# Kernel optimization log

Hardware: AMD Instinct MI355X
Metric: run time of the kernel (lower is better)

The kernel has to match this reference:

```python
import jax, jax.numpy as jnp
import numpy as np

# Dimensions (Gemma-2B-like, uniform q-head rank)
B, S, HID = 2, 2048, 2048
H, HKV, D = 16, 8, 128
RQ, RK, RV = 64, 64, 64
G = H // HKV  # heads per kv group
SCALE = D ** -0.5
NEG_INF = -1e9


def setup_inputs() -> dict:
    key = jax.random.key(0)
    ks = jax.random.split(key, 9)
    hidden_states = jax.random.normal(ks[0], (B, S, HID), dtype=jnp.float32)
    W_A_q = jax.random.normal(ks[1], (H * RQ, HID), dtype=jnp.float32) * 0.02
    W_A_k = jax.random.normal(ks[2], (HKV * RK, HID), dtype=jnp.float32) * 0.02
    W_A_v = jax.random.normal(ks[3], (HKV * RV, HID), dtype=jnp.float32) * 0.02
    B_q = jax.random.normal(ks[4], (H, RQ, D), dtype=jnp.float32)
    B_k = jax.random.normal(ks[5], (HKV, RK, D), dtype=jnp.float32)
    B_v = jax.random.normal(ks[6], (HKV, RV, D), dtype=jnp.float32)
    W_o = jax.random.normal(ks[7], (HID, H * D), dtype=jnp.float32) * 0.02
    # RoPE tables (cos/sin form of gemma's complex freqs_cis)
    inv_freq = 1.0 / (10000.0 ** (jnp.arange(0, D, 2, dtype=jnp.float32) / D))
    freqs = jnp.arange(S, dtype=jnp.float32)[:, None] * inv_freq[None, :]  # [S, D/2]
    freqs_cos = jnp.cos(freqs)
    freqs_sin = jnp.sin(freqs)
    # Causal additive mask [1, 1, S, S]
    causal = jnp.tril(jnp.ones((S, S), dtype=bool))
    mask = jnp.where(causal, 0.0, NEG_INF).astype(jnp.float32)[None, None]
    kv_write_indices = jnp.arange(S, dtype=jnp.int32)
    return {
        'hidden_states': hidden_states, 'W_A_q': W_A_q, 'W_A_k': W_A_k,
        'W_A_v': W_A_v, 'B_q': B_q, 'B_k': B_k, 'B_v': B_v, 'W_o': W_o,
        'freqs_cos': freqs_cos, 'freqs_sin': freqs_sin, 'mask': mask,
        'kv_write_indices': kv_write_indices,
    }


def _rope(x, cos, sin):
    # x: [b, s, h, d]; gemma pairs first half with second half of head_dim
    x1, x2 = jnp.split(x, 2, axis=-1)
    c = cos[None, :, None, :]
    s = sin[None, :, None, :]
    return jnp.concatenate([x1 * c - x2 * s, x1 * s + x2 * c], axis=-1)


def reference(hidden_states, W_A_q, W_A_k, W_A_v, B_q, B_k, B_v, W_o,
              freqs_cos, freqs_sin, mask, kv_write_indices):
    b, s, _ = hidden_states.shape
    # Low-rank A factors
    A_q = jnp.einsum('bsd,rd->bsr', hidden_states, W_A_q).reshape(b, s, H, RQ)
    A_k = jnp.einsum('bsd,rd->bsr', hidden_states, W_A_k).reshape(b, s, HKV, RK)
    A_v = jnp.einsum('bsd,rd->bsr', hidden_states, W_A_v).reshape(b, s, HKV, RV)
    # Factorized KV cache: scatter A factors at write indices (prefill)
    cache_kA = jnp.zeros((b, s, HKV, RK), hidden_states.dtype).at[:, kv_write_indices].set(A_k)
    cache_vA = jnp.zeros((b, s, HKV, RV), hidden_states.dtype).at[:, kv_write_indices].set(A_v)
    # GQA expansion of cached A factors
    gidx = jnp.repeat(jnp.arange(HKV), G)  # [H]
    A_k_rep = cache_kA[:, :, gidx]  # [b, kv, H, RK]
    A_v_rep = cache_vA[:, :, gidx]
    # Reconstruct Q/K/V from constant B factors (per-head loop vectorized:
    # all q ranks equal, so einsum over heads is the same math)
    q = jnp.einsum('bshr,hrd->bshd', A_q, B_q) / RQ
    k = jnp.einsum('bkhr,hrd->bkhd', A_k_rep, B_k[gidx]) / RK
    v = jnp.einsum('bkhr,hrd->bkhd', A_v_rep, B_v[gidx]) / RV
    # RoPE post-reconstruction
    q = _rope(q, freqs_cos, freqs_sin)
    k = _rope(k, freqs_cos, freqs_sin)
    # Attention
    scores = jnp.einsum('bqhd,bkhd->bhqk', q, k) * SCALE + mask
    probs = jax.nn.softmax(scores, axis=-1)
    out = jnp.einsum('bhqk,bkhd->bqhd', probs, v).reshape(b, s, H * D)
    return jnp.einsum('bse,he->bsh', out, W_o)
```

## Files before the change

kernel.cpp:

```cpp
#include <hip/hip_runtime.h>
#include <hip/hip_bf16.h>

typedef __attribute__((ext_vector_type(8))) short bf16x8;
typedef __attribute__((ext_vector_type(4))) float f32x4;

#define MFMA_16x16x32(a,b,c) __builtin_amdgcn_mfma_f32_16x16x32_bf16((a),(b),(c),0,0,0)

__device__ __forceinline__ unsigned short f2b(float f){
  unsigned int u = __builtin_bit_cast(unsigned int, f);
  u = u + 0x7FFFu + ((u >> 16) & 1u);
  return (unsigned short)(u >> 16);
}
__device__ __forceinline__ float b2f(unsigned short h){
  unsigned int u = ((unsigned int)h) << 16;
  return __builtin_bit_cast(float, u);
}

__device__ __forceinline__ void gload_lds16(const unsigned short* g, unsigned short* l){
  __builtin_amdgcn_global_load_lds(
      (const __attribute__((address_space(1))) void*)g,
      (__attribute__((address_space(3))) void*)l, 16, 0, 0);
}


__global__ void cvt_all(const float* __restrict__ hid, const float* __restrict__ wq,
                        const float* __restrict__ wk, const float* __restrict__ wv,
                        const float* __restrict__ wo,
                        unsigned short* __restrict__ Xb, unsigned short* __restrict__ Wqkv,
                        unsigned short* __restrict__ Wob){
  const int N0 = 2097152, N1 = 524288, N2 = 262144, N3 = 262144, N4 = 1048576;
  const int E1 = N0 + N1, E2 = E1 + N2, E3 = E2 + N3, E4 = E3 + N4;
  int i = blockIdx.x * blockDim.x + threadIdx.x;
  const int stride = gridDim.x * blockDim.x;
  for (; i < E4; i += stride){
    const float* s; unsigned short* d; int off;
    if (i < N0)      { s = hid; d = Xb;   off = i; }
    else if (i < E1) { s = wq;  d = Wqkv; off = i - N0; }
    else if (i < E2) { s = wk;  d = Wqkv; off = i - E1 + 524288;  s = wk;  }
    else if (i < E3) { s = wv;  d = Wqkv; off = i - E2 + 786432; }
    else             { s = wo;  d = Wob;  off = i - E3; }
    int src_off = (i < N0) ? i : (i < E1) ? (i - N0) : (i < E2) ? (i - E1) : (i < E3) ? (i - E2) : (i - E3);
    float4 v = reinterpret_cast<const float4*>(s)[src_off];
    ushort4 o;
    o.x = f2b(v.x); o.y = f2b(v.y); o.z = f2b(v.z); o.w = f2b(v.w);
    reinterpret_cast<ushort4*>(d)[off] = o;
  }
}

__global__ void cvt_factors(const float* __restrict__ Bq, const float* __restrict__ Bk,
                            const float* __restrict__ Bv,
                            unsigned short* __restrict__ Bqt, unsigned short* __restrict__ Bkt,
                            unsigned short* __restrict__ Bvt){
  int i = blockIdx.x * blockDim.x + threadIdx.x;
  if (i >= 32*8192) return;
  int H = i >> 13, e = i & 8191;
  int d = e & 127, r = (e >> 7) & 63;
  const float* src; unsigned short* dst; int h;
  if (H < 16)      { src = Bq; dst = Bqt; h = H; }
  else if (H < 24) { src = Bk; dst = Bkt; h = H - 16; }
  else             { src = Bv; dst = Bvt; h = H - 24; }
  dst[(h << 13) + (d << 6) + r] = f2b(src[(size_t)(h << 13) + e]);
}


template<int OUT_F32>
__global__ __launch_bounds__(256) void gemm_bt(
    const unsigned short* __restrict__ A, const unsigned short* __restrict__ B,
    void* __restrict__ Cv, int N, int K, float scale)
{
  __shared__ unsigned short As[2][128*64];
  __shared__ unsigned short Bs[2][128*64];
  const int tid = threadIdx.x;
  const int mb = blockIdx.x, nb = blockIdx.y;
  const int w = tid >> 6, lane = tid & 63;
  const int wr = w >> 1, wc = w & 1;
  const int l16 = lane & 15, lg = lane >> 4;

  f32x4 acc[4][4] = {};

  const unsigned short* Ap = A + (size_t)(mb*128)*K;
  const unsigned short* Bp = B + (size_t)(nb*128)*K;

  const int sRo = 32*w + (lane >> 3);
  const int sCo = ((lane & 7) ^ (lane >> 3)) << 3;
  const int ldsW = 2048*w;

  auto stage = [&](int kt, int buf){
    const unsigned short* Ak = Ap + (size_t)kt*64 + sCo;
    const unsigned short* Bk = Bp + (size_t)kt*64 + sCo;
    #pragma unroll
    for (int i = 0; i < 4; i++)
      gload_lds16(Ak + (size_t)(sRo + 8*i)*K, &As[buf][ldsW + 512*i]);
    #pragma unroll
    for (int i = 0; i < 4; i++)
      gload_lds16(Bk + (size_t)(sRo + 8*i)*K, &Bs[buf][ldsW + 512*i]);
  };

  const int nkt = K >> 6;
  stage(0, 0);
  __syncthreads();

  int cur = 0;
  for (int kt = 0; kt < nkt; kt++){
    if (kt + 1 < nkt) stage(kt + 1, cur ^ 1);
    #pragma unroll
    for (int t = 0; t < 2; t++){
      bf16x8 af[4], bf[4];
      #pragma unroll
      for (int i = 0; i < 4; i++){
        int rowA = wr*64 + i*16 + l16;
        int col  = t*32 + lg*8;
        af[i] = *reinterpret_cast<const bf16x8*>(&As[cur][(rowA*64 + col) ^ ((rowA & 7) << 3)]);
        int rowB = wc*64 + i*16 + l16;
        bf[i] = *reinterpret_cast<const bf16x8*>(&Bs[cur][(rowB*64 + col) ^ ((rowB & 7) << 3)]);
      }
      #pragma unroll
      for (int i = 0; i < 4; i++)
        #pragma unroll
        for (int j = 0; j < 4; j++)
          acc[i][j] = MFMA_16x16x32(af[i], bf[j], acc[i][j]);
    }
    __syncthreads();
    cur ^= 1;
  }

  #pragma unroll
  for (int i = 0; i < 4; i++){
    #pragma unroll
    for (int j = 0; j < 4; j++){
      int row = mb*128 + wr*64 + i*16 + lg*4;
      int col = nb*128 + wc*64 + j*16 + l16;
      #pragma unroll
      for (int r = 0; r < 4; r++){
        float v = acc[i][j][r] * scale;
        if (OUT_F32) reinterpret_cast<float*>(Cv)[(size_t)(row + r)*N + col] = v;
        else reinterpret_cast<unsigned short*>(Cv)[(size_t)(row + r)*N + col] = f2b(v);
      }
    }
  }
}


__global__ __launch_bounds__(256) void factor_rope(
    const unsigned short* __restrict__ A,
    const unsigned short* __restrict__ Bqt, const unsigned short* __restrict__ Bkt,
    const unsigned short* __restrict__ Bvt,
    unsigned short* __restrict__ qb, unsigned short* __restrict__ kb2,
    unsigned short* __restrict__ vb,
    const float* __restrict__ fc, const float* __restrict__ fs)
{
  __shared__ unsigned short As[128*64];
  __shared__ unsigned short Bs[128*64];
  const int tid = threadIdx.x, mb = blockIdx.x, H = blockIdx.y;
  const int w = tid >> 6, lane = tid & 63;
  const int l16 = lane & 15, lg = lane >> 4;
  const float SCALE = 0.08838834764831845f;

  int h, coloff, Hn; const unsigned short* Bt; unsigned short* Out; float scale; bool rope;
  if (H < 16)      { h = H;      coloff = h*64;        Hn = 16; Bt = Bqt + (size_t)h*8192; Out = qb;  scale = SCALE/64.f; rope = true; }
  else if (H < 24) { h = H - 16; coloff = 1024 + h*64; Hn = 8;  Bt = Bkt + (size_t)h*8192; Out = kb2; scale = 1.f/64.f;   rope = true; }
  else             { h = H - 24; coloff = 1536 + h*64; Hn = 8;  Bt = Bvt + (size_t)h*8192; Out = vb;  scale = 1.f/64.f;   rope = false; }

  const int srow = tid >> 3;
  const int scol = (tid & 7) << 3;
  const unsigned short* Ap = A + (size_t)(mb*128)*2048 + coloff;

  #pragma unroll
  for (int c = 0; c < 4; c++){
    int r = srow + 32*c;
    int idx = (r*64 + scol) ^ ((r & 7) << 3);
    *reinterpret_cast<bf16x8*>(&As[idx]) = *reinterpret_cast<const bf16x8*>(Ap + (size_t)r*2048 + scol);
    *reinterpret_cast<bf16x8*>(&Bs[idx]) = *reinterpret_cast<const bf16x8*>(Bt + r*64 + scol);
  }
  __syncthreads();

  f32x4 acc[2][8] = {};
  #pragma unroll
  for (int t = 0; t < 2; t++){
    bf16x8 af[2], bf[8];
    #pragma unroll
    for (int i = 0; i < 2; i++){
      int rowA = w*32 + i*16 + l16;
      int col  = t*32 + lg*8;
      af[i] = *reinterpret_cast<const bf16x8*>(&As[(rowA*64 + col) ^ ((rowA & 7) << 3)]);
    }
    #pragma unroll
    for (int j = 0; j < 8; j++){
      int rowB = j*16 + l16;
      int col  = t*32 + lg*8;
      bf[j] = *reinterpret_cast<const bf16x8*>(&Bs[(rowB*64 + col) ^ ((rowB & 7) << 3)]);
    }
    #pragma unroll
    for (int i = 0; i < 2; i++)
      #pragma unroll
      for (int j = 0; j < 8; j++)
        acc[i][j] = MFMA_16x16x32(af[i], bf[j], acc[i][j]);
  }

  #pragma unroll
  for (int i = 0; i < 2; i++){
    #pragma unroll
    for (int j = 0; j < 4; j++){
      int d = j*16 + l16;
      #pragma unroll
      for (int r = 0; r < 4; r++){
        int row = mb*128 + w*32 + i*16 + lg*4 + r;
        int s = row & 2047, bb = row >> 11;
        float lo = acc[i][j][r] * scale;
        float hi = acc[i][j+4][r] * scale;
        float o1, o2;
        if (rope){
          float cc = fc[(size_t)s*64 + d];
          float ss = fs[(size_t)s*64 + d];
          o1 = lo*cc - hi*ss;
          o2 = lo*ss + hi*cc;
        } else { o1 = lo; o2 = hi; }
        size_t base = ((size_t)(bb*Hn + h)*2048 + s)*128;
        Out[base + d]      = f2b(o1);
        Out[base + 64 + d] = f2b(o2);
      }
    }
  }
}


__device__ __forceinline__ int vt_idx(int d, int kv){
  return d*64 + ((((kv >> 3) + d + (d >> 3)) & 7) << 3) + (kv & 7);
}

__global__ __launch_bounds__(256) void flash_attn(
    const unsigned short* __restrict__ Q,
    const unsigned short* __restrict__ Kb,
    const unsigned short* __restrict__ Vb,
    unsigned short* __restrict__ O)
{
  __shared__ unsigned short Ks[64*128];
  __shared__ unsigned short Vrow[64*128];
  __shared__ unsigned short Vt[128*64];
  __shared__ unsigned short Pl[4][16*64];

  const int tid = threadIdx.x;
  const int w = tid >> 6, lane = tid & 63;
  const int l16 = lane & 15, lg = lane >> 4;
  const int h = blockIdx.y, b = blockIdx.z;
  const int hkv = h >> 1;

  const size_t hbase  = ((size_t)(b*16 + h))*2048*128;
  const size_t kvbase = ((size_t)(b*8 + hkv))*2048*128;

  const int sR = w*16 + (lane >> 4);
  const int sC = (lane & 15) * 8;

  auto stage = [&](int kb){
    #pragma unroll
    for (int i = 0; i < 4; i++){
      int R = sR + i*4;
      const unsigned short* gk = Kb + kvbase + (size_t)(kb*64 + R)*128 + (sC ^ ((R & 7) << 3));
      gload_lds16(gk, &Ks[(w*16 + i*4)*128]);
      const unsigned short* gv = Vb + kvbase + (size_t)(kb*64 + R)*128 + sC;
      gload_lds16(gv, &Vrow[(w*16 + i*4)*128]);
    }
  };

  stage(0);
  __syncthreads();

  const int tkv0 = (tid >> 4) * 4;
  const int td0  = (tid & 15) * 8;

  const int qtiles[2] = { (int)blockIdx.x, 31 - (int)blockIdx.x };

  for (int ph = 0; ph < 2; ph++){
    const int qe = qtiles[ph];
    const size_t qbase = hbase + (size_t)(qe*64 + w*16)*128;
    const int qrow0 = qe*64 + w*16 + lg*4;

    bf16x8 aq[4];
    #pragma unroll
    for (int t = 0; t < 4; t++)
      aq[t] = *reinterpret_cast<const bf16x8*>(&Q[qbase + (size_t)l16*128 + t*32 + lg*8]);

    f32x4 oac[8] = {};
    float mrow[4], lrow[4];
    #pragma unroll
    for (int r = 0; r < 4; r++){ mrow[r] = -1e30f; lrow[r] = 0.f; }

    for (int kb = 0; kb <= qe; kb++){
      bf16x8 vr0 = *reinterpret_cast<const bf16x8*>(&Vrow[(tkv0 + 0)*128 + td0]);
      bf16x8 vr1 = *reinterpret_cast<const bf16x8*>(&Vrow[(tkv0 + 1)*128 + td0]);
      bf16x8 vr2 = *reinterpret_cast<const bf16x8*>(&Vrow[(tkv0 + 2)*128 + td0]);
      bf16x8 vr3 = *reinterpret_cast<const bf16x8*>(&Vrow[(tkv0 + 3)*128 + td0]);

      f32x4 sac[4] = {};
      #pragma unroll
      for (int nt = 0; nt < 4; nt++){
        #pragma unroll
        for (int t = 0; t < 4; t++){
          int rowK = nt*16 + l16;
          int col  = t*32 + lg*8;
          bf16x8 bk = *reinterpret_cast<const bf16x8*>(&Ks[(rowK*128 + col) ^ ((rowK & 7) << 3)]);
          sac[nt] = MFMA_16x16x32(aq[t], bk, sac[nt]);
        }
      }

      #pragma unroll
      for (int j = 0; j < 8; j++){
        unsigned int lo = (unsigned int)(unsigned short)vr0[j] | ((unsigned int)(unsigned short)vr1[j] << 16);
        unsigned int hi = (unsigned int)(unsigned short)vr2[j] | ((unsigned int)(unsigned short)vr3[j] << 16);
        uint2 u; u.x = lo; u.y = hi;
        *reinterpret_cast<uint2*>(&Vt[vt_idx(td0 + j, tkv0)]) = u;
      }

      if (kb == qe){
        #pragma unroll
        for (int nt = 0; nt < 4; nt++){
          int kcol = kb*64 + nt*16 + l16;
          #pragma unroll
          for (int r = 0; r < 4; r++)
            if (kcol > qrow0 + r) sac[nt][r] = -1e30f;
        }
      }
      float corr[4];
      #pragma unroll
      for (int r = 0; r < 4; r++){
        float v = fmaxf(fmaxf(sac[0][r], sac[1][r]), fmaxf(sac[2][r], sac[3][r]));
        v = fmaxf(v, __shfl_xor(v, 1));
        v = fmaxf(v, __shfl_xor(v, 2));
        v = fmaxf(v, __shfl_xor(v, 4));
        v = fmaxf(v, __shfl_xor(v, 8));
        float mn = fmaxf(mrow[r], v);
        corr[r] = __expf(mrow[r] - mn);
        mrow[r] = mn;
      }
      float rs[4] = {0.f, 0.f, 0.f, 0.f};
      #pragma unroll
      for (int nt = 0; nt < 4; nt++){
        #pragma unroll
        for (int r = 0; r < 4; r++){
          float p = __expf(sac[nt][r] - mrow[r]);
          sac[nt][r] = p;
          rs[r] += p;
        }
      }
      #pragma unroll
      for (int r = 0; r < 4; r++){
        float v = rs[r];
        v += __shfl_xor(v, 1); v += __shfl_xor(v, 2); v += __shfl_xor(v, 4); v += __shfl_xor(v, 8);
        lrow[r] = lrow[r]*corr[r] + v;
      }
      #pragma unroll
      for (int dn = 0; dn < 8; dn++)
        #pragma unroll
        for (int r = 0; r < 4; r++) oac[dn][r] *= corr[r];

      #pragma unroll
      for (int nt = 0; nt < 4; nt++){
        #pragma unroll
        for (int r = 0; r < 4; r++){
          int row = lg*4 + r, col = nt*16 + l16;
          Pl[w][(row*64 + col) ^ ((row & 7) << 3)] = f2b(sac[nt][r]);
        }
      }

      __syncthreads();
      if (kb < qe) stage(kb + 1);
      else if (ph == 0) stage(0);

      #pragma unroll
      for (int t = 0; t < 2; t++){
        int colp = t*32 + lg*8;
        bf16x8 ap = *reinterpret_cast<const bf16x8*>(&Pl[w][(l16*64 + colp) ^ ((l16 & 7) << 3)]);
        #pragma unroll
        for (int dn = 0; dn < 8; dn++){
          int rowV = dn*16 + l16;
          bf16x8 bv = *reinterpret_cast<const bf16x8*>(&Vt[vt_idx(rowV, colp)]);
          oac[dn] = MFMA_16x16x32(ap, bv, oac[dn]);
        }
      }
      __syncthreads();
    }

    #pragma unroll
    for (int dn = 0; dn < 8; dn++){
      #pragma unroll
      for (int r = 0; r < 4; r++){
        int row = qe*64 + w*16 + lg*4 + r;
        O[((size_t)(b*2048 + row))*2048 + h*128 + dn*16 + l16] = f2b(oac[dn][r] / lrow[r]);
      }
    }
  }
}


extern "C" void kernel_launch(void* const* d_in, const int* in_sizes, int n_in,
                              void* d_out, int out_size, void* d_ws, size_t ws_size,
                              hipStream_t stream)
{
  if (n_in < 10) return;
  const float* hidden = (const float*)d_in[0];
  const float* WAq = (const float*)d_in[1];
  const float* WAk = (const float*)d_in[2];
  const float* WAv = (const float*)d_in[3];
  const float* Bq  = (const float*)d_in[4];
  const float* Bk  = (const float*)d_in[5];
  const float* Bv  = (const float*)d_in[6];
  const float* Wo  = (const float*)d_in[7];
  const float* fcos = (const float*)d_in[8];
  const float* fsin = (const float*)d_in[9];
  float* out = (float*)d_out;

  char* p = (char*)d_ws;
  auto take = [&](size_t bytes){ char* q = p; p += (bytes + 255) & ~(size_t)255; return q; };
  unsigned short* Xb   = (unsigned short*)take((size_t)4096*2048*2);
  unsigned short* Wqkv = (unsigned short*)take((size_t)2048*2048*2);
  unsigned short* Wob  = (unsigned short*)take((size_t)2048*2048*2);
  unsigned short* Aqkv = (unsigned short*)take((size_t)4096*2048*2);
  unsigned short* Bqt  = (unsigned short*)take((size_t)16*128*64*2);
  unsigned short* Bkt  = (unsigned short*)take((size_t)8*128*64*2);
  unsigned short* Bvt  = (unsigned short*)take((size_t)8*128*64*2);
  unsigned short* qbuf = (unsigned short*)take((size_t)2*16*2048*128*2);
  unsigned short* kbuf = (unsigned short*)take((size_t)2*8*2048*128*2);
  unsigned short* vbuf = (unsigned short*)take((size_t)2*8*2048*128*2);
  unsigned short* aout = (unsigned short*)take((size_t)4096*2048*2);
  if ((size_t)(p - (char*)d_ws) > ws_size) return;

  cvt_all<<<4096, 256, 0, stream>>>(hidden, WAq, WAk, WAv, Wo, Xb, Wqkv, Wob);
  cvt_factors<<<1024, 256, 0, stream>>>(Bq, Bk, Bv, Bqt, Bkt, Bvt);

  gemm_bt<0><<<dim3(32,16), 256, 0, stream>>>(Xb, Wqkv, (void*)Aqkv, 2048, 2048, 1.0f);

  factor_rope<<<dim3(32,32), 256, 0, stream>>>(Aqkv, Bqt, Bkt, Bvt, qbuf, kbuf, vbuf, fcos, fsin);

  flash_attn<<<dim3(16,16,2), 256, 0, stream>>>(qbuf, kbuf, vbuf, aout);

  gemm_bt<1><<<dim3(32,16), 256, 0, stream>>>(aout, Wob, (void*)out, 2048, 2048, 1.0f);
}
```

Measured before the change: 357.9 us.

## Transpose attention MFMA layout so each lane owns one query row

Swaps the MFMA operands in both the QK^T and PV products so the accumulators come out transposed, with each lane holding a single query row. Row max and row sum then need only two cross-lane shuffles instead of four per row, and one scalar m/l replaces four per lane. The log2(e) factor is folded into the Q scale so the softmax can use exp2f. The softmax is moved after the barrier and K/V staging so it overlaps the prefetch, and the output store is vectorized to ushort4. It relies on explicit lgkmcnt waits and sched_barrier to order the P writes to LDS, which adds a risk of ordering mistakes.

```diff
diff --git a/kernel.cpp b/kernel.cpp
--- a/kernel.cpp
+++ b/kernel.cpp
@@ -36,7 +36,7 @@
     const float* s; unsigned short* d; int off;
     if (i < N0)      { s = hid; d = Xb;   off = i; }
     else if (i < E1) { s = wq;  d = Wqkv; off = i - N0; }
-    else if (i < E2) { s = wk;  d = Wqkv; off = i - E1 + 524288;  s = wk;  }
+    else if (i < E2) { s = wk;  d = Wqkv; off = i - E1 + 524288; }
     else if (i < E3) { s = wv;  d = Wqkv; off = i - E2 + 786432; }
     else             { s = wo;  d = Wob;  off = i - E3; }
     int src_off = (i < N0) ? i : (i < E1) ? (i - N0) : (i < E2) ? (i - E1) : (i < E3) ? (i - E2) : (i - E3);
@@ -155,11 +155,12 @@
   const int w = tid >> 6, lane = tid & 63;
   const int l16 = lane & 15, lg = lane >> 4;
   const float SCALE = 0.08838834764831845f;
+  const float LOG2E = 1.4426950408889634f;
 
   int h, coloff, Hn; const unsigned short* Bt; unsigned short* Out; float scale; bool rope;
-  if (H < 16)      { h = H;      coloff = h*64;        Hn = 16; Bt = Bqt + (size_t)h*8192; Out = qb;  scale = SCALE/64.f; rope = true; }
-  else if (H < 24) { h = H - 16; coloff = 1024 + h*64; Hn = 8;  Bt = Bkt + (size_t)h*8192; Out = kb2; scale = 1.f/64.f;   rope = true; }
-  else             { h = H - 24; coloff = 1536 + h*64; Hn = 8;  Bt = Bvt + (size_t)h*8192; Out = vb;  scale = 1.f/64.f;   rope = false; }
+  if (H < 16)      { h = H;      coloff = h*64;        Hn = 16; Bt = Bqt + (size_t)h*8192; Out = qb;  scale = SCALE*LOG2E/64.f; rope = true; }
+  else if (H < 24) { h = H - 16; coloff = 1024 + h*64; Hn = 8;  Bt = Bkt + (size_t)h*8192; Out = kb2; scale = 1.f/64.f;         rope = true; }
+  else             { h = H - 24; coloff = 1536 + h*64; Hn = 8;  Bt = Bvt + (size_t)h*8192; Out = vb;  scale = 1.f/64.f;         rope = false; }
 
   const int srow = tid >> 3;
   const int scol = (tid & 7) << 3;
@@ -273,7 +274,7 @@
   for (int ph = 0; ph < 2; ph++){
     const int qe = qtiles[ph];
     const size_t qbase = hbase + (size_t)(qe*64 + w*16)*128;
-    const int qrow0 = qe*64 + w*16 + lg*4;
+    const int qrow = qe*64 + w*16 + l16;
 
     bf16x8 aq[4];
     #pragma unroll
@@ -281,9 +282,7 @@
       aq[t] = *reinterpret_cast<const bf16x8*>(&Q[qbase + (size_t)l16*128 + t*32 + lg*8]);
 
     f32x4 oac[8] = {};
-    float mrow[4], lrow[4];
-    #pragma unroll
-    for (int r = 0; r < 4; r++){ mrow[r] = -1e30f; lrow[r] = 0.f; }
+    float mreg = -1e30f, lreg = 0.f;
 
     for (int kb = 0; kb <= qe; kb++){
       bf16x8 vr0 = *reinterpret_cast<const bf16x8*>(&Vrow[(tkv0 + 0)*128 + td0]);
@@ -299,7 +298,7 @@
           int rowK = nt*16 + l16;
           int col  = t*32 + lg*8;
           bf16x8 bk = *reinterpret_cast<const bf16x8*>(&Ks[(rowK*128 + col) ^ ((rowK & 7) << 3)]);
-          sac[nt] = MFMA_16x16x32(aq[t], bk, sac[nt]);
+          sac[nt] = MFMA_16x16x32(bk, aq[t], sac[nt]);
         }
       }
 
@@ -314,51 +313,10 @@
       if (kb == qe){
         #pragma unroll
         for (int nt = 0; nt < 4; nt++){
-          int kcol = kb*64 + nt*16 + l16;
+          int k0 = kb*64 + nt*16 + lg*4;
           #pragma unroll
           for (int r = 0; r < 4; r++)
-            if (kcol > qrow0 + r) sac[nt][r] = -1e30f;
-        }
-      }
-      float corr[4];
-      #pragma unroll
-      for (int r = 0; r < 4; r++){
-        float v = fmaxf(fmaxf(sac[0][r], sac[1][r]), fmaxf(sac[2][r], sac[3][r]));
-        v = fmaxf(v, __shfl_xor(v, 1));
-        v = fmaxf(v, __shfl_xor(v, 2));
-        v = fmaxf(v, __shfl_xor(v, 4));
-        v = fmaxf(v, __shfl_xor(v, 8));
-        float mn = fmaxf(mrow[r], v);
-        corr[r] = __expf(mrow[r] - mn);
-        mrow[r] = mn;
-      }
-      float rs[4] = {0.f, 0.f, 0.f, 0.f};
-      #pragma unroll
-      for (int nt = 0; nt < 4; nt++){
-        #pragma unroll
-        for (int r = 0; r < 4; r++){
-          float p = __expf(sac[nt][r] - mrow[r]);
-          sac[nt][r] = p;
-          rs[r] += p;
-        }
-      }
-      #pragma unroll
-      for (int r = 0; r < 4; r++){
-        float v = rs[r];
-        v += __shfl_xor(v, 1); v += __shfl_xor(v, 2); v += __shfl_xor(v, 4); v += __shfl_xor(v, 8);
-        lrow[r] = lrow[r]*corr[r] + v;
-      }
-      #pragma unroll
-      for (int dn = 0; dn < 8; dn++)
-        #pragma unroll
-        for (int r = 0; r < 4; r++) oac[dn][r] *= corr[r];
-
-      #pragma unroll
-      for (int nt = 0; nt < 4; nt++){
-        #pragma unroll
-        for (int r = 0; r < 4; r++){
-          int row = lg*4 + r, col = nt*16 + l16;
-          Pl[w][(row*64 + col) ^ ((row & 7) << 3)] = f2b(sac[nt][r]);
+            if (k0 + r > qrow) sac[nt][r] = -1e30f;
         }
       }
 
@@ -366,27 +324,67 @@
       if (kb < qe) stage(kb + 1);
       else if (ph == 0) stage(0);
 
+      float pm0 = fmaxf(fmaxf(sac[0][0], sac[0][1]), fmaxf(sac[0][2], sac[0][3]));
+      float pm1 = fmaxf(fmaxf(sac[1][0], sac[1][1]), fmaxf(sac[1][2], sac[1][3]));
+      float pm2 = fmaxf(fmaxf(sac[2][0], sac[2][1]), fmaxf(sac[2][2], sac[2][3]));
+      float pm3 = fmaxf(fmaxf(sac[3][0], sac[3][1]), fmaxf(sac[3][2], sac[3][3]));
+      float v = fmaxf(fmaxf(pm0, pm1), fmaxf(pm2, pm3));
+      v = fmaxf(v, __shfl_xor(v, 16));
+      v = fmaxf(v, __shfl_xor(v, 32));
+      float mn = fmaxf(mreg, v);
+      float corr = exp2f(mreg - mn);
+      mreg = mn;
+      float rs = 0.f;
+      #pragma unroll
+      for (int nt = 0; nt < 4; nt++){
+        #pragma unroll
+        for (int r = 0; r < 4; r++){
+          float pp = exp2f(sac[nt][r] - mn);
+          sac[nt][r] = pp;
+          rs += pp;
+        }
+      }
+      rs += __shfl_xor(rs, 16);
+      rs += __shfl_xor(rs, 32);
+      lreg = lreg*corr + rs;
+      #pragma unroll
+      for (int dn = 0; dn < 8; dn++)
+        #pragma unroll
+        for (int r = 0; r < 4; r++) oac[dn][r] *= corr;
+
+      #pragma unroll
+      for (int nt = 0; nt < 4; nt++){
+        #pragma unroll
+        for (int r = 0; r < 4; r++){
+          int k = nt*16 + lg*4 + r;
+          Pl[w][l16*64 + (k ^ ((l16 & 7) << 3))] = f2b(sac[nt][r]);
+        }
+      }
+      asm volatile("s_waitcnt lgkmcnt(0)" ::: "memory");
+      __builtin_amdgcn_sched_barrier(0);
+
       #pragma unroll
       for (int t = 0; t < 2; t++){
-        int colp = t*32 + lg*8;
-        bf16x8 ap = *reinterpret_cast<const bf16x8*>(&Pl[w][(l16*64 + colp) ^ ((l16 & 7) << 3)]);
+        bf16x8 ap = *reinterpret_cast<const bf16x8*>(&Pl[w][l16*64 + ((t*32 + lg*8) ^ ((l16 & 7) << 3))]);
         #pragma unroll
         for (int dn = 0; dn < 8; dn++){
           int rowV = dn*16 + l16;
-          bf16x8 bv = *reinterpret_cast<const bf16x8*>(&Vt[vt_idx(rowV, colp)]);
-          oac[dn] = MFMA_16x16x32(ap, bv, oac[dn]);
+          bf16x8 bv = *reinterpret_cast<const bf16x8*>(&Vt[vt_idx(rowV, t*32 + lg*8)]);
+          oac[dn] = MFMA_16x16x32(bv, ap, oac[dn]);
         }
       }
       __syncthreads();
     }
 
+    float inv = 1.0f / lreg;
     #pragma unroll
     for (int dn = 0; dn < 8; dn++){
-      #pragma unroll
-      for (int r = 0; r < 4; r++){
-        int row = qe*64 + w*16 + lg*4 + r;
-        O[((size_t)(b*2048 + row))*2048 + h*128 + dn*16 + l16] = f2b(oac[dn][r] / lrow[r]);
-      }
+      ushort4 o;
+      o.x = f2b(oac[dn][0] * inv);
+      o.y = f2b(oac[dn][1] * inv);
+      o.z = f2b(oac[dn][2] * inv);
+      o.w = f2b(oac[dn][3] * inv);
+      *reinterpret_cast<ushort4*>(&O[((size_t)(b*2048 + qrow))*2048 + h*128 + dn*16 + lg*4]) = o;
     }
   }
 }
```

After: 358.8 us. About the same (+0.2%).
